# Performance work log

Measured on AMD Instinct MI355X. Metric: run time of the kernel, lower is better.

The kernel has to match this reference:

```python
import jax, jax.numpy as jnp
import numpy as np

LN_EPS = 1e-5


def _layernorm(x, gamma, beta):
    mu = jnp.mean(x, axis=-1, keepdims=True)
    var = jnp.mean(jnp.square(x - mu), axis=-1, keepdims=True)
    return (x - mu) * jax.lax.rsqrt(var + LN_EPS) * gamma + beta


def setup_inputs() -> dict:
    key = jax.random.key(0)
    ks = jax.random.split(key, 8)
    N, E, D = 50000, 800000, 128
    x = jax.random.normal(ks[0], (N, D), dtype=jnp.float32)
    edge_index = jax.random.randint(ks[1], (2, E), 0, N, dtype=jnp.int64)
    edge_weight = jax.random.uniform(ks[2], (E,), dtype=jnp.float32)
    dst_scale = jax.random.uniform(ks[3], (N,), dtype=jnp.float32)
    # learned params: LayerNorm affine + Linear(dim, dim)
    gamma = jnp.ones((D,), dtype=jnp.float32)
    beta = jnp.zeros((D,), dtype=jnp.float32)
    bound = float(np.sqrt(6.0 / (D + D)))  # xavier_uniform
    W = jax.random.uniform(ks[4], (D, D), minval=-bound, maxval=bound, dtype=jnp.float32)
    b = jnp.zeros((D,), dtype=jnp.float32)
    return {"x": x, "gamma": gamma, "beta": beta, "W": W, "b": b,
            "edge_index": edge_index, "num_nodes": N,
            "edge_weight": edge_weight, "dst_scale": dst_scale}


def reference(x, gamma, beta, W, b, edge_index, num_nodes, edge_weight, dst_scale):
    N = int(num_nodes)
    h = _layernorm(x, gamma, beta)            # [N, D]
    m = h @ W.T + b                           # [N, D]
    src = edge_index[0]
    dst = edge_index[1]
    w = edge_weight.astype(jnp.float32)
    msg = m[src] * w[:, None].astype(m.dtype)  # [E, D] gather + weight
    out = jax.ops.segment_sum(msg, dst, num_segments=N)       # scatter-add
    deg = jax.ops.segment_sum(w, dst, num_segments=N)         # weighted degree
    out = out / jnp.maximum(deg, 1.0)[:, None]
    out = out * dst_scale.astype(out.dtype)[:, None]
    y = x + jax.nn.gelu(out, approximate=False)  # dropout=0 -> identity
    return y
```

## Files before the change

kernel.cpp:

```cpp
#include <hip/hip_runtime.h>
#include <hip/hip_bf16.h>
#include <math.h>

typedef __attribute__((ext_vector_type(8))) short short8v;
typedef __attribute__((ext_vector_type(4))) float f32x4;

#define NBUK_MAX 1024
#define CAP      2048
#define CH       6656
#define PUNROLL  26

__global__ __launch_bounds__(256) void prep_kernel(
    const float* __restrict__ W, __hip_bfloat16* __restrict__ Wb,
    int* __restrict__ bcnt)
{
    const int i = blockIdx.x * 256 + threadIdx.x;
    Wb[i] = __float2bfloat16(W[i]);
    if (i < NBUK_MAX) bcnt[i] = 0;
}

__global__ __launch_bounds__(256) void count_kernel(
    const int* __restrict__ ei, int* __restrict__ bcnt, int E, int nbuk)
{
    __shared__ int h[NBUK_MAX];
    for (int j = threadIdx.x; j < nbuk; j += 256) h[j] = 0;
    __syncthreads();
    for (int e = blockIdx.x * 256 + threadIdx.x; e < E; e += gridDim.x * 256)
        atomicAdd(&h[ei[E + e] >> 6], 1);
    __syncthreads();
    for (int j = threadIdx.x; j < nbuk; j += 256)
        if (h[j]) atomicAdd(&bcnt[j], h[j]);
}

__global__ __launch_bounds__(1024) void bscan_kernel(
    const int* __restrict__ bcnt, int* __restrict__ base,
    int* __restrict__ cursor, int nbuk, int E)
{
    __shared__ int sh[1024];
    const int t = threadIdx.x;
    const int v = (t < nbuk) ? bcnt[t] : 0;
    sh[t] = v;
    __syncthreads();
    for (int off = 1; off < 1024; off <<= 1) {
        int u = (t >= off) ? sh[t - off] : 0;
        __syncthreads();
        sh[t] += u;
        __syncthreads();
    }
    const int excl = sh[t] - v;
    if (t < nbuk) { base[t] = excl; cursor[t] = excl; }
    if (t == 0) base[nbuk] = E;
}

__global__ __launch_bounds__(256) void fused_gemm_part_kernel(
    const float* __restrict__ x, const float* __restrict__ gamma,
    const float* __restrict__ beta, const __hip_bfloat16* __restrict__ Wb,
    const float* __restrict__ bias, __hip_bfloat16* __restrict__ m, int N,
    const int* __restrict__ ei, const float* __restrict__ ew,
    int* __restrict__ cursor, uint2* __restrict__ tmp, int E, int nGemm)
{
    __shared__ ushort hlds[4 * 16 * 128];
    __shared__ int ph[NBUK_MAX];
    __shared__ int pb[NBUK_MAX];
    const int tid = threadIdx.x;

    if ((int)blockIdx.x >= nGemm) {
        const int e0 = (blockIdx.x - nGemm) * CH;
        for (int j = tid; j < NBUK_MAX; j += 256) ph[j] = 0;
        __syncthreads();
        int rnk[PUNROLL], dst[PUNROLL];
        #pragma unroll
        for (int i = 0; i < PUNROLL; ++i) {
            const int e = e0 + i * 256 + tid;
            rnk[i] = 0; dst[i] = -1;
            if (e < E) {
                dst[i] = ei[E + e];
                rnk[i] = atomicAdd(&ph[dst[i] >> 6], 1);
            }
        }
        __syncthreads();
        for (int j = tid; j < NBUK_MAX; j += 256)
            pb[j] = ph[j] ? atomicAdd(&cursor[j], ph[j]) : 0;
        __syncthreads();
        #pragma unroll
        for (int i = 0; i < PUNROLL; ++i) {
            const int e = e0 + i * 256 + tid;
            if (e < E) {
                const int d = dst[i];
                const int pos = pb[d >> 6] + rnk[i];
                uint2 kv;
                kv.x = (uint)ei[e] | ((uint)(d & 63) << 16);
                kv.y = __float_as_uint(ew[e]);
                tmp[pos] = kv;
            }
        }
        return;
    }

    const int lane = tid & 63;
    const int wave = tid >> 6;
    const int row0 = blockIdx.x * 64 + wave * 16;
    char* sliceb = (char*)&hlds[wave * 2048];

    const float2 g  = *(const float2*)&gamma[2 * lane];
    const float2 be = *(const float2*)&beta[2 * lane];

    for (int r = 0; r < 16; ++r) {
        const int row = row0 + r;
        float2 v = make_float2(0.0f, 0.0f);
        if (row < N) v = *(const float2*)&x[(size_t)row * 128 + 2 * lane];
        float s = v.x + v.y;
        #pragma unroll
        for (int off = 32; off; off >>= 1) s += __shfl_xor(s, off);
        const float mu = s * 0.0078125f;
        const float d0 = v.x - mu, d1 = v.y - mu;
        float q = d0 * d0 + d1 * d1;
        #pragma unroll
        for (int off = 32; off; off >>= 1) q += __shfl_xor(q, off);
        const float rstd = rsqrtf(q * 0.0078125f + 1e-5f);
        const float h0 = d0 * rstd * g.x + be.x;
        const float h1 = d1 * rstd * g.y + be.y;
        uint packed = (uint)__bfloat16_as_ushort(__float2bfloat16(h0))
                    | ((uint)__bfloat16_as_ushort(__float2bfloat16(h1)) << 16);
        *(uint*)(sliceb + r * 256 + ((lane * 4) ^ ((r & 7) << 4))) = packed;
    }

    const int halfsel = lane >> 4;
    const int jrow    = lane & 15;
    f32x4 acc[8];
    #pragma unroll
    for (int t = 0; t < 8; ++t)
        acc[t] = *(const f32x4*)&bias[t * 16 + halfsel * 4];

    #pragma unroll
    for (int kk = 0; kk < 4; ++kk) {
        const int boff = jrow * 256 + ((kk * 64 + halfsel * 16) ^ ((jrow & 7) << 4));
        short8v hfrag = *(const short8v*)(sliceb + boff);
        #pragma unroll
        for (int t = 0; t < 8; ++t) {
            short8v wfrag = *(const short8v*)&Wb[(size_t)(t * 16 + jrow) * 128
                                                 + kk * 32 + halfsel * 8];
            acc[t] = __builtin_amdgcn_mfma_f32_16x16x32_bf16(wfrag, hfrag, acc[t], 0, 0, 0);
        }
    }

    const int orow = row0 + jrow;
    if (orow < N) {
        #pragma unroll
        for (int t = 0; t < 8; ++t) {
            uint2 o;
            o.x = (uint)__bfloat16_as_ushort(__float2bfloat16(acc[t][0]))
                | ((uint)__bfloat16_as_ushort(__float2bfloat16(acc[t][1])) << 16);
            o.y = (uint)__bfloat16_as_ushort(__float2bfloat16(acc[t][2]))
                | ((uint)__bfloat16_as_ushort(__float2bfloat16(acc[t][3])) << 16);
            *(uint2*)&m[(size_t)orow * 128 + t * 16 + halfsel * 4] = o;
        }
    }
}

__device__ __forceinline__ float gelu_exact(float t) {
    return 0.5f * t * (1.0f + erff(t * 0.70710678118654752f));
}
__device__ __forceinline__ float bf_lo(uint p) {
    return __uint_as_float((p & 0xffffu) << 16);
}
__device__ __forceinline__ float bf_hi(uint p) {
    return __uint_as_float(p & 0xffff0000u);
}

__global__ __launch_bounds__(256) void sortgather_kernel(
    const __hip_bfloat16* __restrict__ m, const int* __restrict__ base,
    const uint2* __restrict__ tmp, const float* __restrict__ x,
    const float* __restrict__ dsc, float* __restrict__ y, int N)
{
    __shared__ uint2 led[CAP];
    __shared__ int hist[64], offs[64], cur[64];
    const int tid = threadIdx.x;
    const int lo  = blockIdx.x * 64;
    const int s0  = base[blockIdx.x];
    const int cnt = base[blockIdx.x + 1] - s0;

    if (tid < 64) { hist[tid] = 0; cur[tid] = 0; }
    __syncthreads();
    for (int i = tid; i < cnt; i += 256)
        atomicAdd(&hist[(tmp[s0 + i].x >> 16) & 63], 1);
    __syncthreads();
    if (tid < 64) {
        const int v = hist[tid];
        int incl = v;
        #pragma unroll
        for (int off = 1; off < 64; off <<= 1) {
            int u = __shfl_up(incl, off);
            if (tid >= off) incl += u;
        }
        offs[tid] = incl - v;
    }
    __syncthreads();
    for (int i = tid; i < cnt; i += 256) {
        const uint2 kv = tmp[s0 + i];
        const int dl = (kv.x >> 16) & 63;
        const int p = offs[dl] + atomicAdd(&cur[dl], 1);
        if (p < CAP) led[p] = kv;
    }
    __syncthreads();

    const int lane = tid & 63;
    const int wv = tid >> 6;
    const uint* mu = (const uint*)m;
    for (int q = 0; q < 16; ++q) {
        const int dl = wv * 16 + q;
        const int d = lo + dl;
        if (d >= N) break;
        const int sA = offs[dl];
        const int eA = min(sA + hist[dl], CAP);
        float ax = 0.0f, ay = 0.0f, deg = 0.0f;
        int j = sA;
        for (; j + 4 <= eA; j += 4) {
            const uint2 k0 = led[j],     k1 = led[j + 1];
            const uint2 k2 = led[j + 2], k3 = led[j + 3];
            const int i0 = k0.x & 0xffff, i1 = k1.x & 0xffff;
            const int i2 = k2.x & 0xffff, i3 = k3.x & 0xffff;
            const float w0 = __uint_as_float(k0.y), w1 = __uint_as_float(k1.y);
            const float w2 = __uint_as_float(k2.y), w3 = __uint_as_float(k3.y);
            const uint p0 = mu[(size_t)i0 * 64 + lane];
            const uint p1 = mu[(size_t)i1 * 64 + lane];
            const uint p2 = mu[(size_t)i2 * 64 + lane];
            const uint p3 = mu[(size_t)i3 * 64 + lane];
            ax = fmaf(w0, bf_lo(p0), ax);  ay = fmaf(w0, bf_hi(p0), ay);
            ax = fmaf(w1, bf_lo(p1), ax);  ay = fmaf(w1, bf_hi(p1), ay);
            ax = fmaf(w2, bf_lo(p2), ax);  ay = fmaf(w2, bf_hi(p2), ay);
            ax = fmaf(w3, bf_lo(p3), ax);  ay = fmaf(w3, bf_hi(p3), ay);
            deg += (w0 + w1) + (w2 + w3);
        }
        for (; j < eA; ++j) {
            const uint2 kv = led[j];
            const float wj = __uint_as_float(kv.y);
            const uint pv = mu[(size_t)(kv.x & 0xffff) * 64 + lane];
            ax = fmaf(wj, bf_lo(pv), ax);
            ay = fmaf(wj, bf_hi(pv), ay);
            deg += wj;
        }
        const float sc = dsc[d] / fmaxf(deg, 1.0f);
        const float2 xv = *(const float2*)&x[(size_t)d * 128 + 2 * lane];
        float2 r;
        r.x = xv.x + gelu_exact(ax * sc);
        r.y = xv.y + gelu_exact(ay * sc);
        *(float2*)&y[(size_t)d * 128 + 2 * lane] = r;
    }
}

extern "C" void kernel_launch(void* const* d_in, const int* in_sizes, int n_in,
                              void* d_out, int out_size, void* d_ws, size_t ws_size,
                              hipStream_t stream) {
    const float* x     = (const float*)d_in[0];
    const float* gamma = (const float*)d_in[1];
    const float* beta  = (const float*)d_in[2];
    const float* W     = (const float*)d_in[3];
    const float* bias  = (const float*)d_in[4];
    const int*   ei    = (const int*)d_in[5];
    const float* ew    = (const float*)d_in[7];
    const float* dsc   = (const float*)d_in[8];

    const int N = in_sizes[0] / 128;
    const int E = in_sizes[5] / 2;
    const int nbuk = (N + 63) / 64;

    float* y = (float*)d_out;

    __hip_bfloat16* m  = (__hip_bfloat16*)d_ws;
    __hip_bfloat16* Wb = m + (size_t)N * 128;
    int*   bcnt   = (int*)(Wb + 16384);
    int*   base   = bcnt + NBUK_MAX;
    int*   cursor = base + NBUK_MAX + 1;
    uint2* tmp    = (uint2*)(cursor + NBUK_MAX);

    prep_kernel<<<64, 256, 0, stream>>>(W, Wb, bcnt);
    count_kernel<<<256, 256, 0, stream>>>(ei, bcnt, E, nbuk);
    bscan_kernel<<<1, 1024, 0, stream>>>(bcnt, base, cursor, nbuk, E);

    const int nGemm = (N + 63) / 64;
    const int nPart = (E + CH - 1) / CH;
    fused_gemm_part_kernel<<<nGemm + nPart, 256, 0, stream>>>(
        x, gamma, beta, Wb, bias, m, N, ei, ew, cursor, tmp, E, nGemm);

    sortgather_kernel<<<nbuk, 256, 0, stream>>>(m, base, tmp, x, dsc, y, N);
}
```

Baseline: 189.7 us.

## Halve destination bucket size to 32 nodes and deepen gather unroll

Destination buckets shrink from 64 to 32 nodes, which doubles the number of sortgather blocks (about 1563) and the bucket count. The bucket scan is rewritten as a wave-shuffle scan over 8 values per thread so it can cover up to 2048 buckets. The gather inner loop is unrolled to 8 independent loads to keep more memory requests in flight. The intent is better occupancy and load balance in the gather phase, at the cost of more partition histogram work and more cursor atomics.

```diff
diff --git a/kernel.cpp b/kernel.cpp
--- a/kernel.cpp
+++ b/kernel.cpp
@@ -5,50 +5,69 @@
 typedef __attribute__((ext_vector_type(8))) short short8v;
 typedef __attribute__((ext_vector_type(4))) float f32x4;
 
-#define NBUK_MAX 1024
-#define CAP      2048
+#define NBUK_CAP 2048
+#define BSH      5
+#define BDST     32
+#define CAP      1024
 #define CH       6656
 #define PUNROLL  26
 
 __global__ __launch_bounds__(256) void prep_kernel(
     const float* __restrict__ W, __hip_bfloat16* __restrict__ Wb,
-    int* __restrict__ bcnt)
+    int* __restrict__ bcnt, int nbuk)
 {
     const int i = blockIdx.x * 256 + threadIdx.x;
     Wb[i] = __float2bfloat16(W[i]);
-    if (i < NBUK_MAX) bcnt[i] = 0;
+    if (i < nbuk) bcnt[i] = 0;
 }
 
 __global__ __launch_bounds__(256) void count_kernel(
     const int* __restrict__ ei, int* __restrict__ bcnt, int E, int nbuk)
 {
-    __shared__ int h[NBUK_MAX];
+    __shared__ int h[NBUK_CAP];
     for (int j = threadIdx.x; j < nbuk; j += 256) h[j] = 0;
     __syncthreads();
     for (int e = blockIdx.x * 256 + threadIdx.x; e < E; e += gridDim.x * 256)
-        atomicAdd(&h[ei[E + e] >> 6], 1);
+        atomicAdd(&h[ei[E + e] >> BSH], 1);
     __syncthreads();
     for (int j = threadIdx.x; j < nbuk; j += 256)
         if (h[j]) atomicAdd(&bcnt[j], h[j]);
 }
 
-__global__ __launch_bounds__(1024) void bscan_kernel(
+__global__ __launch_bounds__(256) void bscan_kernel(
     const int* __restrict__ bcnt, int* __restrict__ base,
     int* __restrict__ cursor, int nbuk, int E)
 {
-    __shared__ int sh[1024];
+    __shared__ int wsum[4];
     const int t = threadIdx.x;
-    const int v = (t < nbuk) ? bcnt[t] : 0;
-    sh[t] = v;
-    __syncthreads();
-    for (int off = 1; off < 1024; off <<= 1) {
-        int u = (t >= off) ? sh[t - off] : 0;
-        __syncthreads();
-        sh[t] += u;
-        __syncthreads();
-    }
-    const int excl = sh[t] - v;
-    if (t < nbuk) { base[t] = excl; cursor[t] = excl; }
+    const int lane = t & 63;
+    const int wave = t >> 6;
+    int v[8];
+    int s = 0;
+    #pragma unroll
+    for (int k = 0; k < 8; ++k) {
+        const int i = t * 8 + k;
+        v[k] = (i < nbuk) ? bcnt[i] : 0;
+        s += v[k];
+    }
+    int incl = s;
+    #pragma unroll
+    for (int off = 1; off < 64; off <<= 1) {
+        int u = __shfl_up(incl, off);
+        if (lane >= off) incl += u;
+    }
+    if (lane == 63) wsum[wave] = incl;
+    __syncthreads();
+    int wpre = 0;
+    #pragma unroll
+    for (int w = 0; w < 4; ++w) if (w < wave) wpre += wsum[w];
+    int e = wpre + incl - s;
+    #pragma unroll
+    for (int k = 0; k < 8; ++k) {
+        const int i = t * 8 + k;
+        if (i < nbuk) { base[i] = e; cursor[i] = e; }
+        e += v[k];
+    }
     if (t == 0) base[nbuk] = E;
 }
 
@@ -57,16 +76,17 @@
     const float* __restrict__ beta, const __hip_bfloat16* __restrict__ Wb,
     const float* __restrict__ bias, __hip_bfloat16* __restrict__ m, int N,
     const int* __restrict__ ei, const float* __restrict__ ew,
-    int* __restrict__ cursor, uint2* __restrict__ tmp, int E, int nGemm)
-{
-    __shared__ ushort hlds[4 * 16 * 128];
-    __shared__ int ph[NBUK_MAX];
-    __shared__ int pb[NBUK_MAX];
+    int* __restrict__ cursor, uint2* __restrict__ tmp, int E, int nGemm,
+    int nbuk)
+{
+    __shared__ char smem[16384];
     const int tid = threadIdx.x;
 
     if ((int)blockIdx.x >= nGemm) {
+        int* ph = (int*)smem;
+        int* pb = ph + NBUK_CAP;
         const int e0 = (blockIdx.x - nGemm) * CH;
-        for (int j = tid; j < NBUK_MAX; j += 256) ph[j] = 0;
+        for (int j = tid; j < nbuk; j += 256) ph[j] = 0;
         __syncthreads();
         int rnk[PUNROLL], dst[PUNROLL];
         #pragma unroll
@@ -75,11 +95,11 @@
             rnk[i] = 0; dst[i] = -1;
             if (e < E) {
                 dst[i] = ei[E + e];
-                rnk[i] = atomicAdd(&ph[dst[i] >> 6], 1);
+                rnk[i] = atomicAdd(&ph[dst[i] >> BSH], 1);
             }
         }
         __syncthreads();
-        for (int j = tid; j < NBUK_MAX; j += 256)
+        for (int j = tid; j < nbuk; j += 256)
             pb[j] = ph[j] ? atomicAdd(&cursor[j], ph[j]) : 0;
         __syncthreads();
         #pragma unroll
@@ -87,9 +107,9 @@
             const int e = e0 + i * 256 + tid;
             if (e < E) {
                 const int d = dst[i];
-                const int pos = pb[d >> 6] + rnk[i];
+                const int pos = pb[d >> BSH] + rnk[i];
                 uint2 kv;
-                kv.x = (uint)ei[e] | ((uint)(d & 63) << 16);
+                kv.x = (uint)ei[e] | ((uint)(d & (BDST - 1)) << 16);
                 kv.y = __float_as_uint(ew[e]);
                 tmp[pos] = kv;
             }
@@ -100,7 +120,7 @@
     const int lane = tid & 63;
     const int wave = tid >> 6;
     const int row0 = blockIdx.x * 64 + wave * 16;
-    char* sliceb = (char*)&hlds[wave * 2048];
+    char* sliceb = smem + wave * 4096;
 
     const float2 g  = *(const float2*)&gamma[2 * lane];
     const float2 be = *(const float2*)&beta[2 * lane];
@@ -174,22 +194,22 @@
     const float* __restrict__ dsc, float* __restrict__ y, int N)
 {
     __shared__ uint2 led[CAP];
-    __shared__ int hist[64], offs[64], cur[64];
+    __shared__ int hist[BDST], offs[BDST], cur[BDST];
     const int tid = threadIdx.x;
-    const int lo  = blockIdx.x * 64;
+    const int lo  = blockIdx.x << BSH;
     const int s0  = base[blockIdx.x];
     const int cnt = base[blockIdx.x + 1] - s0;
 
-    if (tid < 64) { hist[tid] = 0; cur[tid] = 0; }
+    if (tid < BDST) { hist[tid] = 0; cur[tid] = 0; }
     __syncthreads();
     for (int i = tid; i < cnt; i += 256)
-        atomicAdd(&hist[(tmp[s0 + i].x >> 16) & 63], 1);
-    __syncthreads();
-    if (tid < 64) {
+        atomicAdd(&hist[(tmp[s0 + i].x >> 16) & (BDST - 1)], 1);
+    __syncthreads();
+    if (tid < BDST) {
         const int v = hist[tid];
         int incl = v;
         #pragma unroll
-        for (int off = 1; off < 64; off <<= 1) {
+        for (int off = 1; off < BDST; off <<= 1) {
             int u = __shfl_up(incl, off);
             if (tid >= off) incl += u;
         }
@@ -198,7 +218,7 @@
     __syncthreads();
     for (int i = tid; i < cnt; i += 256) {
         const uint2 kv = tmp[s0 + i];
-        const int dl = (kv.x >> 16) & 63;
+        const int dl = (kv.x >> 16) & (BDST - 1);
         const int p = offs[dl] + atomicAdd(&cur[dl], 1);
         if (p < CAP) led[p] = kv;
     }
@@ -207,38 +227,37 @@
     const int lane = tid & 63;
     const int wv = tid >> 6;
     const uint* mu = (const uint*)m;
-    for (int q = 0; q < 16; ++q) {
-        const int dl = wv * 16 + q;
+    for (int q = 0; q < 8; ++q) {
+        const int dl = wv * 8 + q;
         const int d = lo + dl;
         if (d >= N) break;
         const int sA = offs[dl];
         const int eA = min(sA + hist[dl], CAP);
         float ax = 0.0f, ay = 0.0f, deg = 0.0f;
         int j = sA;
-        for (; j + 4 <= eA; j += 4) {
-            const uint2 k0 = led[j],     k1 = led[j + 1];
-            const uint2 k2 = led[j + 2], k3 = led[j + 3];
-            const int i0 = k0.x & 0xffff, i1 = k1.x & 0xffff;
-            const int i2 = k2.x & 0xffff, i3 = k3.x & 0xffff;
-            const float w0 = __uint_as_float(k0.y), w1 = __uint_as_float(k1.y);
-            const float w2 = __uint_as_float(k2.y), w3 = __uint_as_float(k3.y);
-            const uint p0 = mu[(size_t)i0 * 64 + lane];
-            const uint p1 = mu[(size_t)i1 * 64 + lane];
-            const uint p2 = mu[(size_t)i2 * 64 + lane];
-            const uint p3 = mu[(size_t)i3 * 64 + lane];
-            ax = fmaf(w0, bf_lo(p0), ax);  ay = fmaf(w0, bf_hi(p0), ay);
-            ax = fmaf(w1, bf_lo(p1), ax);  ay = fmaf(w1, bf_hi(p1), ay);
-            ax = fmaf(w2, bf_lo(p2), ax);  ay = fmaf(w2, bf_hi(p2), ay);
-            ax = fmaf(w3, bf_lo(p3), ax);  ay = fmaf(w3, bf_hi(p3), ay);
-            deg += (w0 + w1) + (w2 + w3);
+        for (; j + 8 <= eA; j += 8) {
+            uint pv[8];
+            float wj[8];
+            #pragma unroll
+            for (int k = 0; k < 8; ++k) {
+                const uint2 kv = led[j + k];
+                wj[k] = __uint_as_float(kv.y);
+                pv[k] = mu[(size_t)(kv.x & 0xffff) * 64 + lane];
+            }
+            #pragma unroll
+            for (int k = 0; k < 8; ++k) {
+                ax = fmaf(wj[k], bf_lo(pv[k]), ax);
+                ay = fmaf(wj[k], bf_hi(pv[k]), ay);
+                deg += wj[k];
+            }
         }
         for (; j < eA; ++j) {
             const uint2 kv = led[j];
-            const float wj = __uint_as_float(kv.y);
+            const float wl = __uint_as_float(kv.y);
             const uint pv = mu[(size_t)(kv.x & 0xffff) * 64 + lane];
-            ax = fmaf(wj, bf_lo(pv), ax);
-            ay = fmaf(wj, bf_hi(pv), ay);
-            deg += wj;
+            ax = fmaf(wl, bf_lo(pv), ax);
+            ay = fmaf(wl, bf_hi(pv), ay);
+            deg += wl;
         }
         const float sc = dsc[d] / fmaxf(deg, 1.0f);
         const float2 xv = *(const float2*)&x[(size_t)d * 128 + 2 * lane];
@@ -263,25 +282,25 @@
 
     const int N = in_sizes[0] / 128;
     const int E = in_sizes[5] / 2;
-    const int nbuk = (N + 63) / 64;
+    const int nbuk = (N + BDST - 1) / BDST;
 
     float* y = (float*)d_out;
 
     __hip_bfloat16* m  = (__hip_bfloat16*)d_ws;
     __hip_bfloat16* Wb = m + (size_t)N * 128;
     int*   bcnt   = (int*)(Wb + 16384);
-    int*   base   = bcnt + NBUK_MAX;
-    int*   cursor = base + NBUK_MAX + 1;
-    uint2* tmp    = (uint2*)(cursor + NBUK_MAX);
-
-    prep_kernel<<<64, 256, 0, stream>>>(W, Wb, bcnt);
+    int*   base   = bcnt + NBUK_CAP;
+    int*   cursor = base + NBUK_CAP + 1;
+    uint2* tmp    = (uint2*)(cursor + NBUK_CAP);
+
+    prep_kernel<<<64, 256, 0, stream>>>(W, Wb, bcnt, nbuk);
     count_kernel<<<256, 256, 0, stream>>>(ei, bcnt, E, nbuk);
-    bscan_kernel<<<1, 1024, 0, stream>>>(bcnt, base, cursor, nbuk, E);
+    bscan_kernel<<<1, 256, 0, stream>>>(bcnt, base, cursor, nbuk, E);
 
     const int nGemm = (N + 63) / 64;
     const int nPart = (E + CH - 1) / CH;
     fused_gemm_part_kernel<<<nGemm + nPart, 256, 0, stream>>>(
-        x, gamma, beta, Wb, bias, m, N, ei, ew, cursor, tmp, E, nGemm);
+        x, gamma, beta, Wb, bias, m, N, ei, ew, cursor, tmp, E, nGemm, nbuk);
 
     sortgather_kernel<<<nbuk, 256, 0, stream>>>(m, base, tmp, x, dsc, y, N);
 }
```

Result: faster. 177.0 us (-6.7%).
